# Kernel optimization log

Hardware: AMD Instinct MI355X
Metric: run time of the kernel (lower is better)

## Reference

```python
import jax, jax.numpy as jnp
import numpy as np

# hyperparameters matching init_kwargs
SIGMA_COLOR = 1.0 / (1.0 * 1.0 * 2)   # 1/(2*sigma_color^2), sigma_color=1.0
SIGMA_SPACE = 1.0 / (1.0 * 1.0 * 2)   # 1/(2*sigma_space^2), sigma_space=1.0
WINDOW_SIZE = 1                        # 3x3 window
LP = 0.8                               # p_small (Lp norm from paper)
P_LARGE = 2.0                          # p_large for flat regions
C1 = 1.0
C2 = 1.0
EPS = 1e-8


def _window_diffs(img, w):
    """Stack img - shifted(img) over all (2w+1)^2 offsets, reflection padded.
    Faithful to the torch indexing: offset index = (x+w) + (y+w)*(2w+1),
    x applied to the height axis, y to the width axis (H must equal W).
    Returns [B, (2w+1)^2, C, H, W]."""
    B, C, H, W = img.shape
    p = jnp.pad(img, ((0, 0), (0, 0), (w, w), (w, w)), mode='reflect')
    outs = []
    for y in range(-w, w + 1):
        for x in range(-w, w + 1):
            outs.append(img - p[:, :, w + x: w + x + H, w + y: w + y + W])
    return jnp.stack(outs, axis=1)


def _spatial_weights(w, sigma_space, dtype):
    ws = []
    for y in range(-w, w + 1):
        for x in range(-w, w + 1):
            ws.append(np.exp(-sigma_space * (x * x + y * y)))
    return jnp.asarray(np.array(ws, dtype=np.float32), dtype=dtype)  # [(2w+1)^2]


def _edge_response(img):
    """Simple gradient-magnitude edge response, summed over channels. [B,H,W]"""
    p = jnp.pad(img, ((0, 0), (0, 0), (1, 1), (1, 1)), mode='reflect')
    dx = img - p[:, :, 2:, 1:-1]   # vertical neighbor diff
    dy = img - p[:, :, 1:-1, 2:]   # horizontal neighbor diff
    return (dx * dx + dy * dy).sum(axis=1)


def setup_inputs() -> dict:
    key = jax.random.key(0)
    k1, k2 = jax.random.split(key)
    original_images = jax.random.normal(k1, (8, 3, 512, 512), dtype=jnp.float32)
    smooth_images = jax.random.normal(k2, (8, 3, 512, 512), dtype=jnp.float32)
    return {"original_images": original_images, "smooth_images": smooth_images}


def reference(original_images, smooth_images):
    w = WINDOW_SIZE
    # 1. |Ti - Tj| over the (2w+1)^2 window  -> [B, K, C, H, W]
    d = jnp.abs(_window_diffs(smooth_images, w))

    # 2. bilateral color weight wr from original images (3x3 window, hardcoded
    #    window_size=1 in the torch module)  -> [B, 9, 1, H, W]
    diff_o = _window_diffs(original_images, 1)
    wr = jnp.exp((-SIGMA_COLOR * diff_o * diff_o).sum(axis=2, keepdims=True))

    # spatial Gaussian weight ws per offset -> broadcast [1, K, 1, 1, 1]
    ws = _spatial_weights(w, SIGMA_SPACE, d.dtype)[None, :, None, None, None]

    # 3. binary masks from edge responses
    e_orig = _edge_response(original_images)   # [B, H, W]
    e_smooth = _edge_response(smooth_images)
    use_large = ((e_orig < C1) & (e_smooth - e_orig > C2))
    mask_large = use_large[:, None, None, :, :].astype(d.dtype)  # [B,1,1,H,W]

    # masked weighted Lp loss (p_large on flat regions with ws, p_small with wr)
    term_large = ws * jnp.power(d + EPS, P_LARGE)
    term_small = wr * jnp.power(d + EPS, LP)
    loss = jnp.mean(mask_large * term_large + (1.0 - mask_large) * term_small)
    return loss
```

## Files before the change

### kernel.cpp

```cpp
#include <hip/hip_runtime.h>

__device__ __forceinline__ float fexp2(float x) { return __builtin_amdgcn_exp2f(x); }
__device__ __forceinline__ float flog2(float x) { return __builtin_amdgcn_logf(x); }

#define WS1 0.60653065971263342f
#define WS2 0.36787944117144233f

struct PairP { float ps, sq; };

template<int CI, int CJ>
__device__ __forceinline__ PairP pp(const float (&I)[6][4], const float (&J)[6][4], float wsd)
{
    float d0 = I[0][CI] - J[0][CJ], d1 = I[1][CI] - J[1][CJ], d2 = I[2][CI] - J[2][CJ];
    float sO = fmaf(d0, d0, fmaf(d1, d1, d2 * d2));
    float t0 = fabsf(I[3][CI] - J[3][CJ]) + 1e-8f;
    float t1 = fabsf(I[4][CI] - J[4][CJ]) + 1e-8f;
    float t2 = fabsf(I[5][CI] - J[5][CJ]) + 1e-8f;
    PairP r;
    r.ps = fexp2(-0.72134752044448169f * sO) *
           (fexp2(0.8f * flog2(t0)) + fexp2(0.8f * flog2(t1)) + fexp2(0.8f * flog2(t2)));
    r.sq = wsd * fmaf(t0, t0, fmaf(t1, t1, t2 * t2));
    return r;
}

__device__ __forceinline__ void load_row(float R[6][4], const float* const pb[6],
                                         int row, int cm1, int c, int cp1, int cp2)
{
    const int rb = (row > 511 ? 1022 - row : row) << 9;
    #pragma unroll
    for (int p = 0; p < 6; ++p) {
        const float* g = pb[p] + rb;
        R[p][0] = g[cm1]; R[p][1] = g[c]; R[p][2] = g[cp1]; R[p][3] = g[cp2];
    }
}

__device__ __forceinline__ void mask3(float M[3], const float X_[6][4], const float Y_[6][4])
{
    #pragma unroll
    for (int j = 0; j < 3; ++j) {
        float eo = 0.f, es = 0.f;
        #pragma unroll
        for (int p = 0; p < 3; ++p) {
            float a = X_[p][j];
            float d1 = a - Y_[p][j], d2 = a - X_[p][j + 1];
            eo += d1 * d1 + d2 * d2;
            float s = X_[p + 3][j];
            float f1 = s - Y_[p + 3][j], f2 = s - X_[p + 3][j + 1];
            es += f1 * f1 + f2 * f2;
        }
        M[j] = (eo < 1.f && es - eo > 1.f) ? 1.f : 0.f;
    }
}

__device__ __forceinline__ float combine(
    const PairP& pE, const PairP& pS, const PairP& pSE, const PairP& pSW,
    float mi, float mE, float mS, float mSE, float mSW,
    int h, int w, bool border)
{
    float a = fmaf(mi, 3e-16f - 1.1943215e-6f, 1.1943215e-6f);
    if (!border) {
        a += (2.f - mi - mE ) * pE.ps  + (mi + mE ) * pE.sq;
        a += (2.f - mi - mS ) * pS.ps  + (mi + mS ) * pS.sq;
        a += (2.f - mi - mSE) * pSE.ps + (mi + mSE) * pSE.sq;
        a += (2.f - mi - mSW) * pSW.ps + (mi + mSW) * pSW.sq;
    } else {
        float aE = (w == 0)   ? 2.f : 1.f, bE = (w == 510) ? 2.f : 1.f;
        float aS = (h == 0)   ? 2.f : 1.f, bS = (h == 510) ? 2.f : 1.f;
        float aW = (w == 511) ? 2.f : 1.f, bW = (w == 1)   ? 2.f : 1.f;
        bool  vE = (w <= 510), vS = (h <= 510);
        bool  vD = vS && vE,   vW = vS && (w >= 1);
        float cEf = vE ? aE : 0.f,      cEb = vE ? bE : 0.f;
        float cSf = vS ? aS : 0.f,      cSb = vS ? bS : 0.f;
        float cDf = vD ? aS * aE : 0.f, cDb = vD ? bS * bE : 0.f;
        float cWf = vW ? aS * aW : 0.f, cWb = vW ? bS * bW : 0.f;
        a += (fmaf(cEf, -mi, cEf) + fmaf(cEb, -mE,  cEb)) * pE.ps  + fmaf(cEf, mi, cEb * mE ) * pE.sq;
        a += (fmaf(cSf, -mi, cSf) + fmaf(cSb, -mS,  cSb)) * pS.ps  + fmaf(cSf, mi, cSb * mS ) * pS.sq;
        a += (fmaf(cDf, -mi, cDf) + fmaf(cDb, -mSE, cDb)) * pSE.ps + fmaf(cDf, mi, cDb * mSE) * pSE.sq;
        a += (fmaf(cWf, -mi, cWf) + fmaf(cWb, -mSW, cWb)) * pSW.ps + fmaf(cWf, mi, cWb * mSW) * pSW.sq;
    }
    return a;
}

#define MSTEP(B_, C_, N_, S_)                                                   \
    {                                                                           \
        load_row(N_, pb, h0 + (S_) + 2, cm1, c, cp1, cp2);                      \
        PairP pE  = pp<1, 2>(B_, B_, WS1);                                      \
        PairP pS  = pp<1, 1>(B_, C_, WS1);                                      \
        PairP pSE = pp<1, 2>(B_, C_, WS2);                                      \
        PairP pSW = pp<1, 0>(B_, C_, WS2);                                      \
        float mN[3]; mask3(mN, C_, N_);                                         \
        acc += combine(pE, pS, pSE, pSW, mB[1], mB[2], mN[1], mN[2], mN[0],     \
                       h0 + (S_), c, wborder);                                  \
        mB[0] = mN[0]; mB[1] = mN[1]; mB[2] = mN[2];                            \
    }

__global__ __launch_bounds__(256) void smooth_loss_kernel(
    const float* __restrict__ orig, const float* __restrict__ smo,
    float* __restrict__ out)
{
    const int tid  = threadIdx.x;
    const int bid  = blockIdx.x;
    const int b    = bid >> 7;
    const int rem  = bid & 127;
    const int band = rem >> 1;
    const int half = rem & 1;
    const int h0   = band << 3;
    const int c    = (half << 8) | tid;

    const int cm1 = (c == 0)   ? 1   : c - 1;
    const int cp1 = (c == 511) ? 510 : c + 1;
    const int cp2 = (c >= 510) ? 1022 - (c + 2) : c + 2;

    const int wc = (half << 8) | (tid & 192);
    const bool wborder = (band == 0) | (band == 63) | (wc == 0) | (wc == 448);

    const float* pb[6];
    #pragma unroll
    for (int p = 0; p < 3; ++p) {
        pb[p]     = orig + ((b * 3 + p) << 18);
        pb[p + 3] = smo  + ((b * 3 + p) << 18);
    }

    float D0[6][4], D1[6][4], D2[6][4];
    float mB[3];
    float acc = 0.f;

    load_row(D0, pb, h0,     cm1, c, cp1, cp2);
    load_row(D1, pb, h0 + 1, cm1, c, cp1, cp2);
    mask3(mB, D0, D1);

    MSTEP(D0, D1, D2, 0)
    MSTEP(D1, D2, D0, 1)
    MSTEP(D2, D0, D1, 2)
    MSTEP(D0, D1, D2, 3)
    MSTEP(D1, D2, D0, 4)
    MSTEP(D2, D0, D1, 5)
    MSTEP(D0, D1, D2, 6)
    MSTEP(D1, D2, D0, 7)

    acc *= (1.0f / 56623104.0f);

    #pragma unroll
    for (int o = 32; o > 0; o >>= 1)
        acc += __shfl_down(acc, o, 64);

    __shared__ float wsum[4];
    const int lane = tid & 63;
    const int wid  = tid >> 6;
    if (lane == 0) wsum[wid] = acc;
    __syncthreads();
    if (tid == 0)
        atomicAdd(out, wsum[0] + wsum[1] + wsum[2] + wsum[3]);
}

extern "C" void kernel_launch(void* const* d_in, const int* in_sizes, int n_in,
                              void* d_out, int out_size, void* d_ws, size_t ws_size,
                              hipStream_t stream) {
    const float* orig = (const float*)d_in[0];
    const float* smo  = (const float*)d_in[1];
    float* out = (float*)d_out;

    (void)hipMemsetAsync(out, 0, sizeof(float), stream);
    smooth_loss_kernel<<<1024, 256, 0, stream>>>(orig, smo, out);
}
```

Measured before the change: 33.73 us.

## Process two adjacent columns per thread with float2 loads and shorter row bands

Each thread now handles two adjacent columns, using float2 vector loads for the center and right neighbors and sharing the loaded window between both outputs. The band height drops from 8 to 4 rows so the grid stays at 1024 blocks of 256 threads, and one block covers a full 512-wide row band. This cuts scalar loads and redundant neighbor fetches per output pixel, but more bands means more halo rows are reloaded, and register use per thread goes up. The reflect handling at the edges was rewritten (cm1 clamps to 0, c2c clamps to 510), which relies on the border combine logic covering those cases.

```diff
diff --git a/kernel.cpp b/kernel.cpp
--- a/kernel.cpp
+++ b/kernel.cpp
@@ -9,7 +9,7 @@
 struct PairP { float ps, sq; };
 
 template<int CI, int CJ>
-__device__ __forceinline__ PairP pp(const float (&I)[6][4], const float (&J)[6][4], float wsd)
+__device__ __forceinline__ PairP pp(const float (&I)[6][5], const float (&J)[6][5], float wsd)
 {
     float d0 = I[0][CI] - J[0][CJ], d1 = I[1][CI] - J[1][CJ], d2 = I[2][CI] - J[2][CJ];
     float sO = fmaf(d0, d0, fmaf(d1, d1, d2 * d2));
@@ -23,21 +23,25 @@
     return r;
 }
 
-__device__ __forceinline__ void load_row(float R[6][4], const float* const pb[6],
-                                         int row, int cm1, int c, int cp1, int cp2)
+__device__ __forceinline__ void load_row(float R[6][5], const float* const pb[6],
+                                         int row, int cm1, int c0, int c2c)
 {
     const int rb = (row > 511 ? 1022 - row : row) << 9;
     #pragma unroll
     for (int p = 0; p < 6; ++p) {
         const float* g = pb[p] + rb;
-        R[p][0] = g[cm1]; R[p][1] = g[c]; R[p][2] = g[cp1]; R[p][3] = g[cp2];
+        R[p][0] = g[cm1];
+        float2 v0 = *(const float2*)(g + c0);
+        R[p][1] = v0.x; R[p][2] = v0.y;
+        float2 v2 = *(const float2*)(g + c2c);
+        R[p][3] = v2.x; R[p][4] = v2.y;
     }
 }
 
-__device__ __forceinline__ void mask3(float M[3], const float X_[6][4], const float Y_[6][4])
+__device__ __forceinline__ void mask4(float M[4], const float X_[6][5], const float Y_[6][5])
 {
     #pragma unroll
-    for (int j = 0; j < 3; ++j) {
+    for (int j = 0; j < 4; ++j) {
         float eo = 0.f, es = 0.f;
         #pragma unroll
         for (int p = 0; p < 3; ++p) {
@@ -83,15 +87,21 @@
 
 #define MSTEP(B_, C_, N_, S_)                                                   \
     {                                                                           \
-        load_row(N_, pb, h0 + (S_) + 2, cm1, c, cp1, cp2);                      \
-        PairP pE  = pp<1, 2>(B_, B_, WS1);                                      \
-        PairP pS  = pp<1, 1>(B_, C_, WS1);                                      \
-        PairP pSE = pp<1, 2>(B_, C_, WS2);                                      \
-        PairP pSW = pp<1, 0>(B_, C_, WS2);                                      \
-        float mN[3]; mask3(mN, C_, N_);                                         \
-        acc += combine(pE, pS, pSE, pSW, mB[1], mB[2], mN[1], mN[2], mN[0],     \
-                       h0 + (S_), c, wborder);                                  \
-        mB[0] = mN[0]; mB[1] = mN[1]; mB[2] = mN[2];                            \
+        load_row(N_, pb, h0 + (S_) + 2, cm1, c0, c2c);                          \
+        PairP pE0  = pp<1, 2>(B_, B_, WS1);                                     \
+        PairP pE1  = pp<2, 3>(B_, B_, WS1);                                     \
+        PairP pS0  = pp<1, 1>(B_, C_, WS1);                                     \
+        PairP pS1  = pp<2, 2>(B_, C_, WS1);                                     \
+        PairP pSE0 = pp<1, 2>(B_, C_, WS2);                                     \
+        PairP pSE1 = pp<2, 3>(B_, C_, WS2);                                     \
+        PairP pSW0 = pp<1, 0>(B_, C_, WS2);                                     \
+        PairP pSW1 = pp<2, 1>(B_, C_, WS2);                                     \
+        float mN[4]; mask4(mN, C_, N_);                                         \
+        acc += combine(pE0, pS0, pSE0, pSW0, mB[1], mB[2], mN[1], mN[2], mN[0], \
+                       h0 + (S_), c0, wborder);                                 \
+        acc += combine(pE1, pS1, pSE1, pSW1, mB[2], mB[3], mN[2], mN[3], mN[1], \
+                       h0 + (S_), c0 + 1, wborder);                             \
+        mB[0] = mN[0]; mB[1] = mN[1]; mB[2] = mN[2]; mB[3] = mN[3];             \
     }
 
 __global__ __launch_bounds__(256) void smooth_loss_kernel(
@@ -101,18 +111,15 @@
     const int tid  = threadIdx.x;
     const int bid  = blockIdx.x;
     const int b    = bid >> 7;
-    const int rem  = bid & 127;
-    const int band = rem >> 1;
-    const int half = rem & 1;
-    const int h0   = band << 3;
-    const int c    = (half << 8) | tid;
+    const int band = bid & 127;
+    const int h0   = band << 2;
+    const int c0   = tid << 1;
 
-    const int cm1 = (c == 0)   ? 1   : c - 1;
-    const int cp1 = (c == 511) ? 510 : c + 1;
-    const int cp2 = (c >= 510) ? 1022 - (c + 2) : c + 2;
+    const int cm1 = (c0 == 0) ? 0 : c0 - 1;
+    const int c2c = (c0 + 2 > 510) ? 510 : c0 + 2;
 
-    const int wc = (half << 8) | (tid & 192);
-    const bool wborder = (band == 0) | (band == 63) | (wc == 0) | (wc == 448);
+    const int wc = (tid & 192) << 1;
+    const bool wborder = (band == 0) | (band == 127) | (wc == 0) | (wc == 384);
 
     const float* pb[6];
     #pragma unroll
@@ -121,22 +128,18 @@
         pb[p + 3] = smo  + ((b * 3 + p) << 18);
     }
 
-    float D0[6][4], D1[6][4], D2[6][4];
-    float mB[3];
+    float D0[6][5], D1[6][5], D2[6][5];
+    float mB[4];
     float acc = 0.f;
 
-    load_row(D0, pb, h0,     cm1, c, cp1, cp2);
-    load_row(D1, pb, h0 + 1, cm1, c, cp1, cp2);
-    mask3(mB, D0, D1);
+    load_row(D0, pb, h0,     cm1, c0, c2c);
+    load_row(D1, pb, h0 + 1, cm1, c0, c2c);
+    mask4(mB, D0, D1);
 
     MSTEP(D0, D1, D2, 0)
     MSTEP(D1, D2, D0, 1)
     MSTEP(D2, D0, D1, 2)
     MSTEP(D0, D1, D2, 3)
-    MSTEP(D1, D2, D0, 4)
-    MSTEP(D2, D0, D1, 5)
-    MSTEP(D0, D1, D2, 6)
-    MSTEP(D1, D2, D0, 7)
 
     acc *= (1.0f / 56623104.0f);
 
```

Result: no change. 33.30 us (-1.3%).

## Split edge-mask computation into a separate precompute kernel with byte mask

Applied to the files above, without the earlier changes.

Moves the per-pixel edge-response mask out of the loss kernel into its own kernel that writes a uint8 mask to workspace, read back by the loss kernel. This removes the mask arithmetic and its recomputation from the register-heavy loss loop and skips the last row load. The cost is an extra kernel launch and an extra full pass over both input images plus mask traffic.

```diff
diff --git a/kernel.cpp b/kernel.cpp
--- a/kernel.cpp
+++ b/kernel.cpp
@@ -5,6 +5,45 @@
 
 #define WS1 0.60653065971263342f
 #define WS2 0.36787944117144233f
+
+__global__ __launch_bounds__(256) void mask_kernel(
+    const float* __restrict__ orig, const float* __restrict__ smo,
+    unsigned char* __restrict__ mask)
+{
+    const int gid = blockIdx.x * 256 + threadIdx.x;
+    const int b   = gid >> 16;
+    const int rem = gid & 65535;
+    const int h   = rem >> 7;
+    const int w0  = (rem & 127) << 2;
+
+    const int hp = (h == 511) ? 510 : h + 1;
+    const int w4 = (w0 + 4 > 511) ? 510 : w0 + 4;
+
+    float eo0=0,eo1=0,eo2=0,eo3=0, es0=0,es1=0,es2=0,es3=0;
+    #pragma unroll
+    for (int p = 0; p < 6; ++p) {
+        const int ch = (p < 3) ? p : p - 3;
+        const float* g  = ((p < 3) ? orig : smo) + ((b * 3 + ch) << 18);
+        const float* r0 = g + (h  << 9);
+        const float* r1 = g + (hp << 9);
+        float4 a = *(const float4*)(r0 + w0);
+        float  a4 = r0[w4];
+        float4 d = *(const float4*)(r1 + w0);
+        float t, e0=0,e1=0,e2=0,e3=0;
+        t = a.x - d.x; e0 += t*t;  t = a.x - a.y; e0 += t*t;
+        t = a.y - d.y; e1 += t*t;  t = a.y - a.z; e1 += t*t;
+        t = a.z - d.z; e2 += t*t;  t = a.z - a.w; e2 += t*t;
+        t = a.w - d.w; e3 += t*t;  t = a.w - a4;  e3 += t*t;
+        if (p < 3) { eo0+=e0; eo1+=e1; eo2+=e2; eo3+=e3; }
+        else       { es0+=e0; es1+=e1; es2+=e2; es3+=e3; }
+    }
+    uchar4 m;
+    m.x = (eo0 < 1.f && es0-eo0 > 1.f) ? 1 : 0;
+    m.y = (eo1 < 1.f && es1-eo1 > 1.f) ? 1 : 0;
+    m.z = (eo2 < 1.f && es2-eo2 > 1.f) ? 1 : 0;
+    m.w = (eo3 < 1.f && es3-eo3 > 1.f) ? 1 : 0;
+    *(uchar4*)(mask + ((b << 18) | (h << 9) | w0)) = m;
+}
 
 struct PairP { float ps, sq; };
 
@@ -31,24 +70,6 @@
     for (int p = 0; p < 6; ++p) {
         const float* g = pb[p] + rb;
         R[p][0] = g[cm1]; R[p][1] = g[c]; R[p][2] = g[cp1]; R[p][3] = g[cp2];
-    }
-}
-
-__device__ __forceinline__ void mask3(float M[3], const float X_[6][4], const float Y_[6][4])
-{
-    #pragma unroll
-    for (int j = 0; j < 3; ++j) {
-        float eo = 0.f, es = 0.f;
-        #pragma unroll
-        for (int p = 0; p < 3; ++p) {
-            float a = X_[p][j];
-            float d1 = a - Y_[p][j], d2 = a - X_[p][j + 1];
-            eo += d1 * d1 + d2 * d2;
-            float s = X_[p + 3][j];
-            float f1 = s - Y_[p + 3][j], f2 = s - X_[p + 3][j + 1];
-            es += f1 * f1 + f2 * f2;
-        }
-        M[j] = (eo < 1.f && es - eo > 1.f) ? 1.f : 0.f;
     }
 }
 
@@ -81,22 +102,27 @@
     return a;
 }
 
-#define MSTEP(B_, C_, N_, S_)                                                   \
+#define KSTEP(B_, C_, N_, S_, DOLOAD_)                                          \
     {                                                                           \
-        load_row(N_, pb, h0 + (S_) + 2, cm1, c, cp1, cp2);                      \
+        float nl = 0.f, n0 = 0.f, np = 0.f;                                     \
+        if (DOLOAD_) {                                                          \
+            load_row(N_, pb, h0 + (S_) + 2, cm1, c, cp1, cp2);                  \
+            int rr = h0 + (S_) + 2; rr = rr > 511 ? 511 : rr;                   \
+            const unsigned char* mr = mk + (rr << 9);                           \
+            nl = (float)mr[cm1b]; n0 = (float)mr[c]; np = (float)mr[cp1b];      \
+        }                                                                       \
         PairP pE  = pp<1, 2>(B_, B_, WS1);                                      \
         PairP pS  = pp<1, 1>(B_, C_, WS1);                                      \
         PairP pSE = pp<1, 2>(B_, C_, WS2);                                      \
         PairP pSW = pp<1, 0>(B_, C_, WS2);                                      \
-        float mN[3]; mask3(mN, C_, N_);                                         \
-        acc += combine(pE, pS, pSE, pSW, mB[1], mB[2], mN[1], mN[2], mN[0],     \
+        acc += combine(pE, pS, pSE, pSW, miA, miE, m0, mp, ml,                  \
                        h0 + (S_), c, wborder);                                  \
-        mB[0] = mN[0]; mB[1] = mN[1]; mB[2] = mN[2];                            \
+        miA = m0; miE = mp; ml = nl; m0 = n0; mp = np;                          \
     }
 
-__global__ __launch_bounds__(256) void smooth_loss_kernel(
+__global__ __launch_bounds__(256) void loss_kernel(
     const float* __restrict__ orig, const float* __restrict__ smo,
-    float* __restrict__ out)
+    const unsigned char* __restrict__ mask, float* __restrict__ out)
 {
     const int tid  = threadIdx.x;
     const int bid  = blockIdx.x;
@@ -110,6 +136,8 @@
     const int cm1 = (c == 0)   ? 1   : c - 1;
     const int cp1 = (c == 511) ? 510 : c + 1;
     const int cp2 = (c >= 510) ? 1022 - (c + 2) : c + 2;
+    const int cm1b = (c == 0)   ? 0   : c - 1;
+    const int cp1b = (c == 511) ? 511 : c + 1;
 
     const int wc = (half << 8) | (tid & 192);
     const bool wborder = (band == 0) | (band == 63) | (wc == 0) | (wc == 448);
@@ -120,23 +148,26 @@
         pb[p]     = orig + ((b * 3 + p) << 18);
         pb[p + 3] = smo  + ((b * 3 + p) << 18);
     }
+    const unsigned char* mk = mask + (b << 18);
 
     float D0[6][4], D1[6][4], D2[6][4];
-    float mB[3];
     float acc = 0.f;
 
     load_row(D0, pb, h0,     cm1, c, cp1, cp2);
     load_row(D1, pb, h0 + 1, cm1, c, cp1, cp2);
-    mask3(mB, D0, D1);
+    const unsigned char* mr0 = mk + (h0 << 9);
+    const unsigned char* mr1 = mk + ((h0 + 1) << 9);
+    float miA = (float)mr0[c],    miE = (float)mr0[cp1b];
+    float ml  = (float)mr1[cm1b], m0  = (float)mr1[c], mp = (float)mr1[cp1b];
 
-    MSTEP(D0, D1, D2, 0)
-    MSTEP(D1, D2, D0, 1)
-    MSTEP(D2, D0, D1, 2)
-    MSTEP(D0, D1, D2, 3)
-    MSTEP(D1, D2, D0, 4)
-    MSTEP(D2, D0, D1, 5)
-    MSTEP(D0, D1, D2, 6)
-    MSTEP(D1, D2, D0, 7)
+    KSTEP(D0, D1, D2, 0, 1)
+    KSTEP(D1, D2, D0, 1, 1)
+    KSTEP(D2, D0, D1, 2, 1)
+    KSTEP(D0, D1, D2, 3, 1)
+    KSTEP(D1, D2, D0, 4, 1)
+    KSTEP(D2, D0, D1, 5, 1)
+    KSTEP(D0, D1, D2, 6, 1)
+    KSTEP(D1, D2, D0, 7, 0)
 
     acc *= (1.0f / 56623104.0f);
 
@@ -159,7 +190,9 @@
     const float* orig = (const float*)d_in[0];
     const float* smo  = (const float*)d_in[1];
     float* out = (float*)d_out;
+    unsigned char* mask = (unsigned char*)d_ws;
 
     (void)hipMemsetAsync(out, 0, sizeof(float), stream);
-    smooth_loss_kernel<<<1024, 256, 0, stream>>>(orig, smo, out);
+    mask_kernel<<<2048, 256, 0, stream>>>(orig, smo, mask);
+    loss_kernel<<<1024, 256, 0, stream>>>(orig, smo, mask, out);
 }
```

Result: slower. 42.83 us (+27.0%).
